# Optimization experiments

Measured on AMD Instinct MI355X. Metric: run time of the kernel, lower is better.

## Reference

```python
import jax, jax.numpy as jnp
import numpy as np
from jax import lax

B, A, H, W = 4, 9, 128, 128
FEAT_STRIDE = 16
PRE_NMS_TOPN = 4000
POST_NMS_TOPN = 1000
NMS_THRESH = 0.7
IM_SIZE = 2048.0


def _generate_anchors(base_size=16, ratios=(0.5, 1.0, 2.0), scales=(8.0, 16.0, 32.0)):
    base = np.array([1.0, 1.0, base_size, base_size], dtype=np.float32) - 1.0

    def whctrs(a):
        w = a[2] - a[0] + 1.0
        h = a[3] - a[1] + 1.0
        return w, h, a[0] + 0.5 * (w - 1.0), a[1] + 0.5 * (h - 1.0)

    def mk(ws, hs, xc, yc):
        ws = ws[:, None]
        hs = hs[:, None]
        return np.hstack([xc - 0.5 * (ws - 1.0), yc - 0.5 * (hs - 1.0),
                          xc + 0.5 * (ws - 1.0), yc + 0.5 * (hs - 1.0)])

    w, h, xc, yc = whctrs(base)
    size = w * h
    r = np.array(ratios, dtype=np.float32)
    ws = np.round(np.sqrt(size / r))
    hs = np.round(ws * r)
    ratio_anchors = mk(ws, hs, xc, yc)
    out = []
    s = np.array(scales, dtype=np.float32)
    for a in ratio_anchors:
        w2, h2, xc2, yc2 = whctrs(a)
        out.append(mk(w2 * s, h2 * s, xc2, yc2))
    return np.vstack(out).astype(np.float32)  # [A, 4]


ANCHORS = jnp.asarray(_generate_anchors(FEAT_STRIDE))


def setup_inputs() -> dict:
    key = jax.random.key(0)
    k1, k2 = jax.random.split(key)
    scores = jax.random.normal(k1, (B, 2 * A, H, W), dtype=jnp.float32)
    bbox_deltas = jax.random.normal(k2, (B, 4 * A, H, W), dtype=jnp.float32) * 0.5
    im_info = jnp.tile(jnp.array([IM_SIZE, IM_SIZE, 1.0], dtype=jnp.float32), (B, 1))
    valid_range = jnp.tile(jnp.array([0.0, 10000.0], dtype=jnp.float32), (B, 1))
    return {"scores": scores, "bbox_deltas": bbox_deltas, "im_info": im_info,
            "valid_range": valid_range}


def _bbox_transform_inv(anchors, deltas):
    # anchors [N,4] broadcast against deltas [B,N,4]
    w = anchors[..., 2] - anchors[..., 0] + 1.0
    h = anchors[..., 3] - anchors[..., 1] + 1.0
    cx = anchors[..., 0] + 0.5 * w
    cy = anchors[..., 1] + 0.5 * h
    dx, dy, dw, dh = deltas[..., 0], deltas[..., 1], deltas[..., 2], deltas[..., 3]
    pcx = dx * w + cx
    pcy = dy * h + cy
    pw = jnp.exp(dw) * w
    ph = jnp.exp(dh) * h
    return jnp.stack([pcx - 0.5 * pw, pcy - 0.5 * ph,
                      pcx + 0.5 * pw, pcy + 0.5 * ph], axis=-1)


def _clip_boxes(boxes, im_hw):
    # boxes [B,N,4]; im_hw [B,2] = (height, width)
    boxes = jnp.maximum(boxes, 0.0)
    hmax = im_hw[:, 0][:, None] - 1.0
    wmax = im_hw[:, 1][:, None] - 1.0
    return jnp.stack([jnp.minimum(boxes[..., 0], wmax),
                      jnp.minimum(boxes[..., 1], hmax),
                      jnp.minimum(boxes[..., 2], wmax),
                      jnp.minimum(boxes[..., 3], hmax)], axis=-1)


def _iou_matrix(boxes):
    # boxes [N,4], +1 pixel convention (matches gpu_nms)
    x1, y1, x2, y2 = boxes[:, 0], boxes[:, 1], boxes[:, 2], boxes[:, 3]
    areas = (x2 - x1 + 1.0) * (y2 - y1 + 1.0)
    iw = jnp.maximum(jnp.minimum(x2[:, None], x2[None, :]) - jnp.maximum(x1[:, None], x1[None, :]) + 1.0, 0.0)
    ih = jnp.maximum(jnp.minimum(y2[:, None], y2[None, :]) - jnp.maximum(y1[:, None], y1[None, :]) + 1.0, 0.0)
    inter = iw * ih
    return inter / (areas[:, None] + areas[None, :] - inter)


def _nms_single(proposals, scores_flat):
    # proposals [KA,4], scores_flat [KA] -> [POST,4] zero-padded, score-ordered
    _, order = lax.top_k(scores_flat, PRE_NMS_TOPN)
    boxes = proposals[order]  # [PRE,4] sorted by descending score
    sup_mat = lax.stop_gradient(_iou_matrix(boxes) > NMS_THRESH)
    idxs = jnp.arange(PRE_NMS_TOPN)

    def body(i, supp):
        row = sup_mat[i] & (idxs > i)
        return jnp.where(supp[i], supp, supp | row)

    supp = lax.fori_loop(0, PRE_NMS_TOPN, body, jnp.zeros(PRE_NMS_TOPN, dtype=bool))
    keep = ~supp
    # stable argsort puts kept indices first, preserving score order
    kidx = jnp.argsort(jnp.where(keep, 0, 1), stable=True)[:POST_NMS_TOPN]
    valid = (jnp.arange(POST_NMS_TOPN) < keep.sum()).astype(boxes.dtype)
    return boxes[kidx] * valid[:, None]


def reference(scores, bbox_deltas, im_info, valid_range):
    fg = scores[:, A:, :, :]                      # [B,A,Hf,Wf] objectness scores
    Bc, _, Hf, Wf = fg.shape
    # anchor grid: [K,4] shifts + [A,4] base anchors -> [K*A,4]
    sx = jnp.arange(Wf, dtype=jnp.float32) * FEAT_STRIDE
    sy = jnp.arange(Hf, dtype=jnp.float32) * FEAT_STRIDE
    gx, gy = jnp.meshgrid(sx, sy)                 # [Hf,Wf] (xy indexing like np.meshgrid)
    shifts = jnp.stack([gx.ravel(), gy.ravel(), gx.ravel(), gy.ravel()], axis=1)  # [K,4]
    anchors = (ANCHORS[None, :, :] + shifts[:, None, :]).reshape(-1, 4)           # [K*A,4]

    deltas = bbox_deltas.transpose(0, 2, 3, 1).reshape(Bc, -1, 4)  # [B,K*A,4]
    sc = fg.transpose(0, 2, 3, 1).reshape(Bc, -1)                   # [B,K*A]

    proposals = _bbox_transform_inv(anchors[None, :, :], deltas)
    proposals = _clip_boxes(proposals, im_info[:, :2])

    # filter_proposal_by_range: area = w*h (no +1), score -> -1 if out of range
    widths = proposals[..., 2] - proposals[..., 0]
    heights = proposals[..., 3] - proposals[..., 1]
    area = widths * heights
    min_a = (valid_range[:, 0] ** 2)[:, None]
    max_a = (valid_range[:, 1] ** 2)[:, None]
    sc = jnp.where((area < min_a) | (area > max_a), -1.0, sc)

    out_boxes = jax.vmap(_nms_single)(proposals, sc)  # [B,POST,4]
    batch_col = jnp.broadcast_to(
        jnp.arange(Bc, dtype=out_boxes.dtype)[:, None, None], (Bc, POST_NMS_TOPN, 1))
    return jnp.concatenate([batch_col, out_boxes], axis=-1)  # [B,POST,5]
```

## Files before the change

kernel.cpp:

```cpp
#include <hip/hip_runtime.h>
#include <cmath>

#define WD 128
#define HT 128
#define HW 16384
#define NB 4
#define NA 9
#define NPB (NA*HW)
#define TOPN 4000
#define POSTN 1000
#define CANDCAP 8192
#define REPCAP 1024
#define NREPL 32
#define MROWS 4096
#define RST 4160
#define NTILE 63
#define TRI (NTILE*(NTILE+1)/2)
#define NREP 4
#define PBLK 576
#define NBINS 4096
#define NBLK 42

typedef unsigned long long u64;
typedef unsigned int u32;

struct Anchors { float v[36]; };

static void gen_anchors(float* out) {
    double base[4] = {0.0, 0.0, 15.0, 15.0};
    const double ratios[3] = {0.5, 1.0, 2.0};
    const double scales[3] = {8.0, 16.0, 32.0};
    double w = base[2] - base[0] + 1.0;
    double h = base[3] - base[1] + 1.0;
    double xc = base[0] + 0.5 * (w - 1.0);
    double yc = base[1] + 0.5 * (h - 1.0);
    double size = w * h;
    double ra[3][4];
    for (int r = 0; r < 3; ++r) {
        double ws = nearbyint(sqrt(size / ratios[r]));
        double hs = nearbyint(ws * ratios[r]);
        ra[r][0] = xc - 0.5 * (ws - 1.0);
        ra[r][1] = yc - 0.5 * (hs - 1.0);
        ra[r][2] = xc + 0.5 * (ws - 1.0);
        ra[r][3] = yc + 0.5 * (hs - 1.0);
    }
    int k = 0;
    for (int r = 0; r < 3; ++r) {
        double w2 = ra[r][2] - ra[r][0] + 1.0;
        double h2 = ra[r][3] - ra[r][1] + 1.0;
        double x2c = ra[r][0] + 0.5 * (w2 - 1.0);
        double y2c = ra[r][1] + 0.5 * (h2 - 1.0);
        for (int s = 0; s < 3; ++s) {
            double ws = w2 * scales[s], hs = h2 * scales[s];
            out[k*4+0] = (float)(x2c - 0.5 * (ws - 1.0));
            out[k*4+1] = (float)(y2c - 0.5 * (hs - 1.0));
            out[k*4+2] = (float)(x2c + 0.5 * (ws - 1.0));
            out[k*4+3] = (float)(y2c + 0.5 * (hs - 1.0));
            ++k;
        }
    }
}

__device__ __forceinline__ u32 sortable_key(float sc) {
    u32 sb = __float_as_uint(sc);
    return sb ^ ((sb & 0x80000000u) ? 0xFFFFFFFFu : 0x80000000u);
}

__device__ __forceinline__ u64 readlane64(u64 v, int l) {
    u32 lo = (u32)__builtin_amdgcn_readlane((int)(u32)v, l);
    u32 hi = (u32)__builtin_amdgcn_readlane((int)(u32)(v >> 32), l);
    return ((u64)hi << 32) | lo;
}

__device__ __forceinline__ u64 wave_or64_dpp(u64 v) {
    u32 lo = (u32)v, hi = (u32)(v >> 32);
#define DPPOR(x, ctrl) x |= (u32)__builtin_amdgcn_update_dpp(0, (int)(x), ctrl, 0xf, 0xf, false)
    DPPOR(lo, 0x111); DPPOR(lo, 0x112); DPPOR(lo, 0x114); DPPOR(lo, 0x118);
    DPPOR(lo, 0x142); DPPOR(lo, 0x143);
    DPPOR(hi, 0x111); DPPOR(hi, 0x112); DPPOR(hi, 0x114); DPPOR(hi, 0x118);
    DPPOR(hi, 0x142); DPPOR(hi, 0x143);
#undef DPPOR
    u32 rlo = (u32)__builtin_amdgcn_readlane((int)lo, 63);
    u32 rhi = (u32)__builtin_amdgcn_readlane((int)hi, 63);
    return ((u64)rhi << 32) | rlo;
}

__device__ __forceinline__ float4 decode_box(const float* __restrict__ deltas,
                                             const float* __restrict__ im_info,
                                             const Anchors& A, int b, int a, int p)
{
#pragma clang fp contract(off)
    int hh = p >> 7;
    int ww = p & 127;
    float sx = (float)(ww * 16);
    float sy = (float)(hh * 16);
    float ax1 = A.v[a*4+0] + sx;
    float ay1 = A.v[a*4+1] + sy;
    float ax2 = A.v[a*4+2] + sx;
    float ay2 = A.v[a*4+3] + sy;
    const float* dbase = deltas + ((size_t)(b*36 + a*4))*HW + p;
    float dx = dbase[0];
    float dy = dbase[HW];
    float dw = dbase[2*HW];
    float dh = dbase[3*HW];
    float aw = ax2 - ax1 + 1.0f;
    float ah = ay2 - ay1 + 1.0f;
    float cx = ax1 + 0.5f*aw;
    float cy = ay1 + 0.5f*ah;
    float pcx = dx*aw + cx;
    float pcy = dy*ah + cy;
    float ew = (float)exp((double)dw);
    float eh = (float)exp((double)dh);
    float pw = ew * aw;
    float ph = eh * ah;
    float x1 = pcx - 0.5f*pw;
    float y1 = pcy - 0.5f*ph;
    float x2 = pcx + 0.5f*pw;
    float y2 = pcy + 0.5f*ph;
    float hmax = im_info[b*3+0] - 1.0f;
    float wmax = im_info[b*3+1] - 1.0f;
    x1 = fmaxf(x1, 0.0f); y1 = fmaxf(y1, 0.0f);
    x2 = fmaxf(x2, 0.0f); y2 = fmaxf(y2, 0.0f);
    x1 = fminf(x1, wmax); y1 = fminf(y1, hmax);
    x2 = fminf(x2, wmax); y2 = fminf(y2, hmax);
    return make_float4(x1, y1, x2, y2);
}

__global__ void k_props(const float* __restrict__ scores,
                        const float* __restrict__ deltas,
                        const float* __restrict__ im_info,
                        const float* __restrict__ valid_range,
                        Anchors A,
                        u32* __restrict__ fkeys,
                        u32* __restrict__ hist12)
{
#pragma clang fp contract(off)
    __shared__ u32 lh[NBINS];
    int tid = threadIdx.x;
#pragma unroll
    for (int i = 0; i < NBINS/256; ++i) lh[tid + i*256] = 0;
    __syncthreads();

    int n = blockIdx.x * 256 + tid;
    int b = n / NPB;
    int r = n - b*NPB;
    int a = r / HW;
    int p = r - a*HW;

    float4 bx = decode_box(deltas, im_info, A, b, a, p);
    float sc = scores[((size_t)(b*18 + 9 + a))*HW + p];
    float area = (bx.z - bx.x) * (bx.w - bx.y);
    float v0 = valid_range[b*2+0], v1 = valid_range[b*2+1];
    if (area < v0*v0 || area > v1*v1) sc = -1.0f;

    u32 key = sortable_key(sc);
    fkeys[n] = key;
    atomicAdd(&lh[key >> 20], 1u);
    __syncthreads();

    int rep = blockIdx.x & (NREP-1);
    u32* gh = hist12 + ((size_t)rep*NB + b)*NBINS;
#pragma unroll
    for (int i = 0; i < NBINS/256; ++i) {
        u32 v = lh[tid + i*256];
        if (v) atomicAdd(&gh[tid + i*256], v);
    }
}

__global__ void k_findT(const u32* __restrict__ hist12, u32* __restrict__ thresh12)
{
    __shared__ u32 sfx[1024];
    int b = blockIdx.x, t = threadIdx.x;
    u32 bin0 = 0, bin1 = 0, bin2 = 0, bin3 = 0;
    for (int rr = 0; rr < NREP; ++rr) {
        const u32* h = hist12 + ((size_t)rr*NB + b)*NBINS + t*4;
        bin0 += h[0]; bin1 += h[1]; bin2 += h[2]; bin3 += h[3];
    }
    u32 s4 = bin0 + bin1 + bin2 + bin3;
    sfx[t] = s4;
    __syncthreads();
    for (int d = 1; d < 1024; d <<= 1) {
        u32 add = (t + d < 1024) ? sfx[t + d] : 0u;
        __syncthreads();
        sfx[t] += add;
        __syncthreads();
    }
    u32 above = (t < 1023) ? sfx[t+1] : 0u;
    u32 c3 = bin3 + above;
    u32 c2 = bin2 + c3;
    u32 c1 = bin1 + c2;
    u32 c0 = bin0 + c1;
    if (c3 >= TOPN && above < TOPN) thresh12[b] = (u32)(t*4 + 3);
    if (c2 >= TOPN && c3    < TOPN) thresh12[b] = (u32)(t*4 + 2);
    if (c1 >= TOPN && c2    < TOPN) thresh12[b] = (u32)(t*4 + 1);
    if (c0 >= TOPN && c1    < TOPN) thresh12[b] = (u32)(t*4 + 0);
}

__global__ void k_emit(const u32* __restrict__ fkeys,
                       const u32* __restrict__ thresh12,
                       u32* __restrict__ ccntRep,
                       u64* __restrict__ cand)
{
    int tid = threadIdx.x;
    int n = blockIdx.x * 256 + tid;
    int b = n / NPB;
    int r = n - b*NPB;
    int a = r / HW;
    int p = r - a*HW;
    u32 key = fkeys[n];
    bool cond = (key >> 20) >= thresh12[b];
    u64 m = __ballot(cond);
    int lane = tid & 63;
    int rep = blockIdx.x & (NREPL-1);
    if (cond) {
        int leader = __ffsll((unsigned long long)m) - 1;
        u32 base = 0;
        if (lane == leader)
            base = atomicAdd(&ccntRep[(b*NREPL + rep)*16], (u32)__popcll(m));
        base = (u32)__shfl((int)base, leader);
        u32 pos = base + (u32)__popcll(m & ((1ull << lane) - 1ull));
        if (pos < REPCAP) {
            u32 t = (u32)(p*NA + a);
            cand[((size_t)b*NREPL + rep)*REPCAP + pos] = ((u64)key << 32) | (u32)(~t);
        }
    }
}

__global__ void k_rank2(const u64* __restrict__ cand, const u32* __restrict__ ccntRep,
                        const float* __restrict__ deltas,
                        const float* __restrict__ im_info,
                        Anchors A,
                        float4* __restrict__ topk)
{
    __shared__ u64 kk[CANDCAP];
    __shared__ u32 ps[256];
    __shared__ u32 rcnt[32];
    __shared__ u32 roff[33];
    int b = blockIdx.y;
    int tid = threadIdx.x;
    if (tid < 32) {
        u32 c = ccntRep[(b*NREPL + tid)*16];
        rcnt[tid] = (c > REPCAP) ? REPCAP : c;
    }
    __syncthreads();
    if (tid == 0) {
        u32 acc = 0;
        for (int i = 0; i < 32; ++i) { roff[i] = acc; acc += rcnt[i]; }
        roff[32] = (acc > CANDCAP) ? CANDCAP : acc;
    }
    __syncthreads();
    u32 N = roff[32];
    if ((u32)(blockIdx.x * 64) >= N) return;
    for (int rr = 0; rr < 32; ++rr) {
        u32 len = rcnt[rr], base = roff[rr];
        const u64* src = cand + ((size_t)b*NREPL + rr)*REPCAP;
        for (u32 i = tid; i < len; i += 256) {
            u32 g = base + i;
            if (g < CANDCAP) kk[g] = src[i];
        }
    }
    __syncthreads();
    int kl = tid & 63, seg = tid >> 6;
    u32 ki = (u32)(blockIdx.x * 64 + kl);
    u64 mykey = (ki < N) ? kk[ki] : ~0ull;
    u32 segN = (N + 3) >> 2;
    u32 s0 = seg * segN;
    u32 s1 = s0 + segN; if (s1 > N) s1 = N;
    u32 pr = 0;
    u32 i = s0;
    for (; i + 16 <= s1; i += 16) {
        u64 v0 = kk[i+0],  v1 = kk[i+1],  v2 = kk[i+2],  v3 = kk[i+3];
        u64 v4 = kk[i+4],  v5 = kk[i+5],  v6 = kk[i+6],  v7 = kk[i+7];
        u64 v8 = kk[i+8],  v9 = kk[i+9],  va = kk[i+10], vb = kk[i+11];
        u64 vc = kk[i+12], vd = kk[i+13], ve = kk[i+14], vf = kk[i+15];
        pr += (v0 > mykey) + (v1 > mykey) + (v2 > mykey) + (v3 > mykey);
        pr += (v4 > mykey) + (v5 > mykey) + (v6 > mykey) + (v7 > mykey);
        pr += (v8 > mykey) + (v9 > mykey) + (va > mykey) + (vb > mykey);
        pr += (vc > mykey) + (vd > mykey) + (ve > mykey) + (vf > mykey);
    }
    for (; i < s1; ++i) pr += (kk[i] > mykey) ? 1u : 0u;
    ps[tid] = pr;
    __syncthreads();
    if (seg == 0 && ki < N) {
        u32 rank = ps[kl] + ps[kl+64] + ps[kl+128] + ps[kl+192];
        if (rank < TOPN) {
            u32 t = ~((u32)mykey);
            int a = (int)(t % 9u);
            int p = (int)(t / 9u);
            topk[(size_t)b*MROWS + rank] = decode_box(deltas, im_info, A, b, a, p);
        }
    }
}

__global__ void k_mask(const float4* __restrict__ topk, u64* __restrict__ masksT)
{
#pragma clang fp contract(off)
    int L = blockIdx.x;
    int b = blockIdx.y;
    int ti = (int)((2.0*NTILE + 1.0 -
                    sqrt((2.0*NTILE + 1.0)*(2.0*NTILE + 1.0) - 8.0*(double)L)) * 0.5);
    while ((ti+1)*NTILE - ((ti+1)*ti)/2 <= L) ++ti;
    while (ti*NTILE - (ti*(ti-1))/2 > L) --ti;
    int tj = ti + (L - (ti*NTILE - (ti*(ti-1))/2));

    int r = threadIdx.x;
    int i = ti*64 + r;
    __shared__ float4 cb[64];
    __shared__ float  ca[64];
    u64 word = 0;
    {
        int jj = tj*64 + r;
        float4 cbox = (jj < TOPN) ? topk[(size_t)b*MROWS + jj] : make_float4(0,0,0,0);
        cb[r] = cbox;
        ca[r] = (cbox.z - cbox.x + 1.0f) * (cbox.w - cbox.y + 1.0f);
        __syncthreads();
        if (i < TOPN) {
            float4 rb = topk[(size_t)b*MROWS + i];
            float rarea = (rb.z - rb.x + 1.0f) * (rb.w - rb.y + 1.0f);
            for (int q = 0; q < 64; ++q) {
                float4 cc = cb[q];
                float iw = fminf(rb.z, cc.z) - fmaxf(rb.x, cc.x) + 1.0f;
                float ih = fminf(rb.w, cc.w) - fmaxf(rb.y, cc.y) + 1.0f;
                iw = fmaxf(iw, 0.0f); ih = fmaxf(ih, 0.0f);
                float inter = iw * ih;
                float uni = (rarea + ca[q]) - inter;
                float iou = inter / uni;
                if (iou > 0.7f) word |= (1ULL << q);
            }
            int nvalid = TOPN - tj*64;
            if (nvalid < 64) word &= ((1ULL << nvalid) - 1ULL);
            if (ti == tj) {
                u64 cm = (r == 63) ? ~0ULL : ((1ULL << (r + 1)) - 1ULL);
                word &= ~cm;
            }
        }
    }
    masksT[((size_t)(b*64 + tj))*RST + i] = word;
}

#define NMS_PLOAD(cc) { \
    int cm = ((cc) > 62) ? 62 : (cc); \
    const u64* colp = mb + (size_t)cm*RST; \
    _Pragma("unroll") \
    for (int k = 0; k < NBLK; ++k) \
        if (k <= cm) pf[k] = colp[(size_t)k*64 + lane]; \
}

#define NMS_PSTORE(cc) { \
    int cm = ((cc) > 62) ? 62 : (cc); \
    int wmax = (cm < NBLK-1) ? cm+1 : NBLK; \
    _Pragma("unroll") \
    for (int k = 0; k < NBLK; ++k) \
        if (k < wmax) colbuf[k*64 + lane] = pf[k]; \
}

__global__ __launch_bounds__(64, 1) void k_nms(const u64* __restrict__ masksT,
                      const float4* __restrict__ topk,
                      float* __restrict__ out)
{
    int b = blockIdx.x;
    int lane = threadIdx.x;

    __shared__ u64 colbuf[NBLK*64];
    __shared__ u32 kmexp[64][64];
    __shared__ u64 kmw[64];

    kmw[lane] = 0ull;
#pragma unroll
    for (int k = 0; k < 64; ++k) kmexp[k][lane] = 0u;

    {
        float* ob = out + (size_t)b*POSTN*5;
        for (int e = lane; e < POSTN*5; e += 64)
            ob[e] = ((e % 5) == 0) ? (float)b : 0.0f;
    }

    const u64* mb = masksT + (size_t)b*64*RST;

    u64 pf[NBLK];
    NMS_PLOAD(0)
    NMS_PSTORE(0)
    NMS_PLOAD(1)

    int kcnt = 0;
    for (int c = 0; c < 63; ++c) {
        u64 acc = 0;
        int kmax = (c < NBLK) ? c : NBLK;
#pragma unroll 8
        for (int k = 0; k < kmax; ++k) {
            u32 mk = kmexp[k][lane];
            u64 v = colbuf[k*64 + lane];
            acc |= v & (((u64)mk << 32) | mk);
        }
        for (int k = NBLK; k < c; ++k) {
            u32 mk = kmexp[k][lane];
            u64 v = mb[(size_t)c*RST + (size_t)k*64 + lane];
            acc |= v & (((u64)mk << 32) | mk);
        }
        u64 w = wave_or64_dpp(acc);
        u64 D = (c < NBLK) ? colbuf[c*64 + lane]
                           : mb[(size_t)c*RST + (size_t)c*64 + lane];
#pragma unroll
        for (int r = 0; r < 64; ++r) {
            u64 dr = readlane64(D, r);
            u64 t;
            asm("s_lshr_b64 %[t], %[w], %[rr]\n\t"
                "s_and_b64 %[t], %[t], 1\n\t"
                "s_cselect_b64 %[t], 0, %[d]\n\t"
                "s_or_b64 %[w], %[w], %[t]"
                : [w]"+s"(w), [t]"=&s"(t)
                : [d]"s"(dr), [rr]"i"(r)
                : "scc");
        }
        u64 kmask = ~w & ((c < 62) ? ~0ull : 0xFFFFFFFFull);
        kcnt += __popcll(kmask);
        if (lane == 0) kmw[c] = kmask;
        kmexp[c][lane] = ((u32)((kmask >> lane) & 1ull)) ? ~0u : 0u;

        if (kcnt >= POSTN || c == 62) break;
        NMS_PSTORE(c+1)
        NMS_PLOAD(c+2)
    }

    u64 keepw = kmw[lane];
    int cnt = __popcll(keepw);
    int pre = cnt;
    for (int d = 1; d < 64; d <<= 1) {
        int t = __shfl_up(pre, d);
        if (lane >= d) pre += t;
    }
    int excl = pre - cnt;
    asm volatile("s_waitcnt vmcnt(0)" ::: "memory");
    u64 wv = keepw; int rk = excl;
    while (wv) {
        int bpos = __ffsll((unsigned long long)wv) - 1;
        wv &= wv - 1;
        if (rk < POSTN) {
            int i = lane*64 + bpos;
            float4 bx = topk[(size_t)b*MROWS + i];
            float* o = out + ((size_t)b*POSTN + rk)*5;
            o[1] = bx.x; o[2] = bx.y; o[3] = bx.z; o[4] = bx.w;
        }
        ++rk;
    }
}

extern "C" void kernel_launch(void* const* d_in, const int* in_sizes, int n_in,
                              void* d_out, int out_size, void* d_ws, size_t ws_size,
                              hipStream_t stream)
{
    const float* scores  = (const float*)d_in[0];
    const float* deltas  = (const float*)d_in[1];
    const float* im_info = (const float*)d_in[2];
    const float* vrange  = (const float*)d_in[3];
    float* out = (float*)d_out;

    char* ws = (char*)d_ws;
    size_t off = 0;
    auto alloc = [&](size_t bytes) -> void* {
        void* ptr = ws + off;
        off += (bytes + 255) & ~(size_t)255;
        return ptr;
    };
    u32*   fkeys   = (u32*)   alloc((size_t)NB*NPB*sizeof(u32));
    u64*   cand    = (u64*)   alloc((size_t)NB*NREPL*REPCAP*sizeof(u64));
    float4* topk   = (float4*)alloc((size_t)NB*MROWS*sizeof(float4));
    u64*   masksT  = (u64*)   alloc((size_t)NB*64*RST*sizeof(u64));
    u32*   hist12  = (u32*)   alloc((size_t)NREP*NB*NBINS*sizeof(u32));
    u32*   ccntRep = (u32*)   alloc((size_t)NB*NREPL*16*sizeof(u32));
    u32*   thresh12= (u32*)   alloc(256);

    Anchors A;
    gen_anchors(A.v);

    size_t zbytes = (char*)ccntRep + (size_t)NB*NREPL*16*sizeof(u32) - (char*)hist12;
    hipMemsetAsync(hist12, 0, zbytes, stream);

    int total = NB*NPB;
    int blocks = (total + 255)/256;
    k_props<<<blocks, 256, 0, stream>>>(scores, deltas, im_info, vrange, A, fkeys, hist12);
    k_findT<<<NB, 1024, 0, stream>>>(hist12, thresh12);
    k_emit<<<blocks, 256, 0, stream>>>(fkeys, thresh12, ccntRep, cand);
    dim3 rgrid(CANDCAP/64, NB);
    k_rank2<<<rgrid, 256, 0, stream>>>(cand, ccntRep, deltas, im_info, A, topk);
    dim3 mgrid(TRI, NB);
    k_mask<<<mgrid, 64, 0, stream>>>(topk, masksT);
    k_nms<<<NB, 64, 0, stream>>>(masksT, topk, out);
}
```

Measured before the change: 134.3 us.

## Split NMS sweep into producer and consumer waves with double-buffered columns

The serial NMS kernel now runs two wavefronts per batch. One wave prefetches the next mask column into a double-buffered LDS slot and precomputes the partial OR over all previously finalized blocks. The other wave only folds in the latest block and runs the scalar intra-tile suppression chain. This takes the suppression accumulation and the column loading off the serial critical path, at the cost of two block-wide barriers per column step and a shared exit flag.

```diff
diff --git a/kernel.cpp b/kernel.cpp
--- a/kernel.cpp
+++ b/kernel.cpp
@@ -17,7 +17,6 @@
 #define NTILE 63
 #define TRI (NTILE*(NTILE+1)/2)
 #define NREP 4
-#define PBLK 576
 #define NBINS 4096
 #define NBLK 42
 
@@ -346,102 +345,140 @@
         if (k <= cm) pf[k] = colp[(size_t)k*64 + lane]; \
 }
 
-#define NMS_PSTORE(cc) { \
+#define NMS_PSTORE(cc, BUF) { \
     int cm = ((cc) > 62) ? 62 : (cc); \
     int wmax = (cm < NBLK-1) ? cm+1 : NBLK; \
     _Pragma("unroll") \
     for (int k = 0; k < NBLK; ++k) \
-        if (k < wmax) colbuf[k*64 + lane] = pf[k]; \
-}
-
-__global__ __launch_bounds__(64, 1) void k_nms(const u64* __restrict__ masksT,
+        if (k < wmax) (BUF)[k*64 + lane] = pf[k]; \
+}
+
+__global__ __launch_bounds__(128, 1) void k_nms(const u64* __restrict__ masksT,
                       const float4* __restrict__ topk,
                       float* __restrict__ out)
 {
     int b = blockIdx.x;
-    int lane = threadIdx.x;
-
-    __shared__ u64 colbuf[NBLK*64];
+    int tid = threadIdx.x;
+    int lane = tid & 63;
+    int wid = tid >> 6;
+
+    __shared__ u64 colbuf[2][NBLK*64];
     __shared__ u32 kmexp[64][64];
     __shared__ u64 kmw[64];
-
-    kmw[lane] = 0ull;
+    __shared__ u64 wcomm[1];
+    __shared__ int exitf;
+
+    if (wid == 0) {
+        kmw[lane] = 0ull;
 #pragma unroll
-    for (int k = 0; k < 64; ++k) kmexp[k][lane] = 0u;
-
-    {
+        for (int k = 0; k < 32; ++k) kmexp[k][lane] = 0u;
+    } else {
+#pragma unroll
+        for (int k = 32; k < 64; ++k) kmexp[k][lane] = 0u;
+    }
+    if (tid == 0) { wcomm[0] = 0ull; exitf = 0; }
+
+    const u64* mb = masksT + (size_t)b*64*RST;
+
+    u64 pf[NBLK];
+    u64 accp = 0;
+
+    if (wid == 0) {
         float* ob = out + (size_t)b*POSTN*5;
         for (int e = lane; e < POSTN*5; e += 64)
             ob[e] = ((e % 5) == 0) ? (float)b : 0.0f;
-    }
-
-    const u64* mb = masksT + (size_t)b*64*RST;
-
-    u64 pf[NBLK];
-    NMS_PLOAD(0)
-    NMS_PSTORE(0)
-    NMS_PLOAD(1)
+    } else {
+        NMS_PLOAD(0)
+        NMS_PSTORE(0, colbuf[0])
+        NMS_PLOAD(1)
+    }
 
     int kcnt = 0;
     for (int c = 0; c < 63; ++c) {
-        u64 acc = 0;
-        int kmax = (c < NBLK) ? c : NBLK;
-#pragma unroll 8
-        for (int k = 0; k < kmax; ++k) {
-            u32 mk = kmexp[k][lane];
-            u64 v = colbuf[k*64 + lane];
-            acc |= v & (((u64)mk << 32) | mk);
-        }
-        for (int k = NBLK; k < c; ++k) {
-            u32 mk = kmexp[k][lane];
-            u64 v = mb[(size_t)c*RST + (size_t)k*64 + lane];
-            acc |= v & (((u64)mk << 32) | mk);
-        }
-        u64 w = wave_or64_dpp(acc);
-        u64 D = (c < NBLK) ? colbuf[c*64 + lane]
-                           : mb[(size_t)c*RST + (size_t)c*64 + lane];
+        int cur = c & 1;
+        __syncthreads();
+        if (exitf) break;
+        if (wid == 1) {
+            u64 acc = accp;
+            if (c > 0) {
+                u32 mk = kmexp[c-1][lane];
+                u64 v = (c-1 < NBLK) ? colbuf[cur][(c-1)*64 + lane]
+                                     : mb[(size_t)c*RST + (size_t)(c-1)*64 + lane];
+                acc |= v & (((u64)mk << 32) | mk);
+                for (int k = NBLK; k < c-1; ++k) {
+                    u32 m2 = kmexp[k][lane];
+                    u64 v2 = mb[(size_t)c*RST + (size_t)k*64 + lane];
+                    acc |= v2 & (((u64)m2 << 32) | m2);
+                }
+            }
+            u64 wv = wave_or64_dpp(acc);
+            if (lane == 0) wcomm[0] = wv;
+        }
+        __syncthreads();
+        if (wid == 0) {
+            u64 wl = wcomm[0];
+            u32 wlo = (u32)__builtin_amdgcn_readfirstlane((int)(u32)wl);
+            u32 whi = (u32)__builtin_amdgcn_readfirstlane((int)(u32)(wl >> 32));
+            u64 w = ((u64)whi << 32) | wlo;
+            u64 D = (c < NBLK) ? colbuf[cur][c*64 + lane]
+                               : mb[(size_t)c*RST + (size_t)c*64 + lane];
 #pragma unroll
-        for (int r = 0; r < 64; ++r) {
-            u64 dr = readlane64(D, r);
-            u64 t;
-            asm("s_lshr_b64 %[t], %[w], %[rr]\n\t"
-                "s_and_b64 %[t], %[t], 1\n\t"
-                "s_cselect_b64 %[t], 0, %[d]\n\t"
-                "s_or_b64 %[w], %[w], %[t]"
-                : [w]"+s"(w), [t]"=&s"(t)
-                : [d]"s"(dr), [rr]"i"(r)
-                : "scc");
-        }
-        u64 kmask = ~w & ((c < 62) ? ~0ull : 0xFFFFFFFFull);
-        kcnt += __popcll(kmask);
-        if (lane == 0) kmw[c] = kmask;
-        kmexp[c][lane] = ((u32)((kmask >> lane) & 1ull)) ? ~0u : 0u;
-
-        if (kcnt >= POSTN || c == 62) break;
-        NMS_PSTORE(c+1)
-        NMS_PLOAD(c+2)
-    }
-
-    u64 keepw = kmw[lane];
-    int cnt = __popcll(keepw);
-    int pre = cnt;
-    for (int d = 1; d < 64; d <<= 1) {
-        int t = __shfl_up(pre, d);
-        if (lane >= d) pre += t;
-    }
-    int excl = pre - cnt;
-    asm volatile("s_waitcnt vmcnt(0)" ::: "memory");
-    u64 wv = keepw; int rk = excl;
-    while (wv) {
-        int bpos = __ffsll((unsigned long long)wv) - 1;
-        wv &= wv - 1;
-        if (rk < POSTN) {
-            int i = lane*64 + bpos;
-            float4 bx = topk[(size_t)b*MROWS + i];
-            float* o = out + ((size_t)b*POSTN + rk)*5;
-            o[1] = bx.x; o[2] = bx.y; o[3] = bx.z; o[4] = bx.w;
-        }
-        ++rk;
+            for (int r = 0; r < 64; ++r) {
+                u64 dr = readlane64(D, r);
+                u64 t;
+                asm("s_lshr_b64 %[t], %[w], %[rr]\n\t"
+                    "s_and_b64 %[t], %[t], 1\n\t"
+                    "s_cselect_b64 %[t], 0, %[d]\n\t"
+                    "s_or_b64 %[w], %[w], %[t]"
+                    : [w]"+s"(w), [t]"=&s"(t)
+                    : [d]"s"(dr), [rr]"i"(r)
+                    : "scc");
+            }
+            u64 kmask = ~w & ((c < 62) ? ~0ull : 0xFFFFFFFFull);
+            kcnt += __popcll(kmask);
+            if (lane == 0) {
+                kmw[c] = kmask;
+                if (kcnt >= POSTN || c == 62) exitf = 1;
+            }
+            kmexp[c][lane] = ((u32)((kmask >> lane) & 1ull)) ? ~0u : 0u;
+        } else {
+            NMS_PSTORE(c+1, colbuf[cur^1])
+            u64 ap = 0;
+            int km = (c < NBLK) ? c : NBLK;
+#pragma unroll
+            for (int k = 0; k < NBLK; ++k) {
+                if (k < km) {
+                    u32 mk = kmexp[k][lane];
+                    ap |= pf[k] & (((u64)mk << 32) | mk);
+                }
+            }
+            accp = ap;
+            NMS_PLOAD(c+2)
+        }
+    }
+
+    if (wid == 0) {
+        u64 keepw = kmw[lane];
+        int cnt = __popcll(keepw);
+        int pre = cnt;
+        for (int d = 1; d < 64; d <<= 1) {
+            int t = __shfl_up(pre, d);
+            if (lane >= d) pre += t;
+        }
+        int excl = pre - cnt;
+        asm volatile("s_waitcnt vmcnt(0)" ::: "memory");
+        u64 wv = keepw; int rk = excl;
+        while (wv) {
+            int bpos = __ffsll((unsigned long long)wv) - 1;
+            wv &= wv - 1;
+            if (rk < POSTN) {
+                int i = lane*64 + bpos;
+                float4 bx = topk[(size_t)b*MROWS + i];
+                float* o = out + ((size_t)b*POSTN + rk)*5;
+                o[1] = bx.x; o[2] = bx.y; o[3] = bx.z; o[4] = bx.w;
+            }
+            ++rk;
+        }
     }
 }
 
@@ -485,5 +522,5 @@
     k_rank2<<<rgrid, 256, 0, stream>>>(cand, ccntRep, deltas, im_info, A, topk);
     dim3 mgrid(TRI, NB);
     k_mask<<<mgrid, 64, 0, stream>>>(topk, masksT);
-    k_nms<<<NB, 64, 0, stream>>>(masksT, topk, out);
-}
+    k_nms<<<NB, 128, 0, stream>>>(masksT, topk, out);
+}
```

After: 124.3 us. 7.4% less time.
